# Optimization experiments

Hardware: AMD Instinct MI355X
Metric: run time of the kernel (lower is better)

Reference implementation:

```python
import jax, jax.numpy as jnp
import numpy as np

B, C, H, W = 4, 256, 64, 64
GROUPS = 32
EPS = 1e-5


def setup_inputs() -> dict:
    key = jax.random.key(0)
    ks = jax.random.split(key, 8)
    s = 1.0 / np.sqrt(C)
    return {
        "Hand": jax.random.normal(ks[0], (B, C, H, W), jnp.float32),
        "U": jax.random.normal(ks[1], (B, C, H, W), jnp.float32),
        "WH_w": jax.random.normal(ks[2], (C, C), jnp.float32) * s,
        "WH_b": jax.random.normal(ks[3], (C,), jnp.float32) * 0.01,
        "WU_w": jax.random.normal(ks[4], (C, C), jnp.float32) * s,
        "WU_b": jax.random.normal(ks[5], (C,), jnp.float32) * 0.01,
        "gn_w": jax.random.normal(ks[6], (C,), jnp.float32) * 0.1,
        "gn_b": jax.random.normal(ks[7], (C,), jnp.float32) * 0.1,
    }


def _group_norm(x, w, b):
    # x: [B, C, H, W], normalize within each of GROUPS channel groups over (C//G, H, W)
    b_, c_, h_, w_ = x.shape
    xg = x.reshape(b_, GROUPS, c_ // GROUPS, h_, w_)
    mean = jnp.mean(xg, axis=(2, 3, 4), keepdims=True)
    var = jnp.var(xg, axis=(2, 3, 4), keepdims=True)
    xn = ((xg - mean) * jax.lax.rsqrt(var + EPS)).reshape(b_, c_, h_, w_)
    return xn * w[None, :, None, None] + b[None, :, None, None]


def reference(Hand, U, WH_w, WH_b, WU_w, WU_b, gn_w, gn_b):
    b_, c_, h_, w_ = Hand.shape
    n = h_ * w_
    Hf = Hand.reshape(b_, c_, n)  # [B, C, N]
    Uf = U.reshape(b_, c_, n)     # [B, C, N]
    # 1x1 convs == per-pixel linear on channels
    q = jnp.einsum('oc,bcn->bon', WH_w, Hf) + WH_b[None, :, None]  # [B, C, N]
    k = jnp.einsum('oc,bcn->bon', WU_w, Uf) + WU_b[None, :, None]  # [B, C, N]
    # affinity: A[b, n, m] = sum_c q[b,c,n] * k[b,c,m]  (unscaled)
    A = jnp.einsum('bcn,bcm->bnm', q, k)  # [B, N, N]
    A = jax.nn.softmax(A, axis=-1)
    out = jnp.einsum('bnm,bcm->bcn', A, Uf).reshape(b_, c_, h_, w_)
    return _group_norm(out, gn_w, gn_b) + Hand
```

## Files before the change

### kernel.cpp

```cpp
#include <hip/hip_runtime.h>
#include <hip/hip_fp16.h>
#include <math.h>


typedef _Float16 v8h __attribute__((ext_vector_type(8)));
typedef float    v4f __attribute__((ext_vector_type(4)));

#define NB 4
#define NC 256
#define NS 4096
#define NG 32
#define GEPS 1e-5f
#define NSPLIT 3
#define KSTRIDE 272
#define KTILE   8704
#define PSTRIDE 40

#define ASYNC_BARRIER() asm volatile("s_waitcnt lgkmcnt(0)\n\ts_barrier" ::: "memory")

template <int CTRL>
__device__ __forceinline__ float dpp_rot(float x) {
    int r = __builtin_amdgcn_update_dpp(__float_as_int(x), __float_as_int(x),
                                        CTRL, 0xF, 0xF, false);
    return __int_as_float(r);
}
__device__ __forceinline__ float row_max16(float x) {
    x = fmaxf(x, dpp_rot<0x128>(x));
    x = fmaxf(x, dpp_rot<0x124>(x));
    x = fmaxf(x, dpp_rot<0x122>(x));
    x = fmaxf(x, dpp_rot<0x121>(x));
    return x;
}
__device__ __forceinline__ float row_sum16(float x) {
    x = x + dpp_rot<0x128>(x);
    x = x + dpp_rot<0x124>(x);
    x = x + dpp_rot<0x122>(x);
    x = x + dpp_rot<0x121>(x);
    return x;
}

__global__ __launch_bounds__(256) void k_convert(const float* __restrict__ Wh,
    const float* __restrict__ Wu, _Float16* __restrict__ Wh16, _Float16* __restrict__ Wu16)
{
    const int i = blockIdx.x * 256 + threadIdx.x;
    const int o = i >> 8, c = i & 255;
    const int idx = ((((o >> 4) * 8 + (c >> 5)) * 4 + ((c >> 3) & 3)) * 16
                     + (o & 15)) * 8 + (c & 7);
    Wh16[idx] = (_Float16)Wh[i];
    Wu16[idx] = (_Float16)Wu[i];
}

__global__ __launch_bounds__(256) void k_qkgemm(const float* __restrict__ Hand,
    const float* __restrict__ U, const _Float16* __restrict__ Wh16,
    const _Float16* __restrict__ Wu16, const float* __restrict__ WHb,
    const float* __restrict__ WUb, _Float16* __restrict__ qT,
    _Float16* __restrict__ kTsw, _Float16* __restrict__ Uh)
{
    const int nt = blockIdx.x, b = blockIdx.y, z = blockIdx.z;
    const float*    X    = z ? U    : Hand;
    const _Float16* W    = z ? Wu16 : Wh16;
    const float*    bias = z ? WUb  : WHb;

    const int tid = threadIdx.x, w = tid >> 6, lane = tid & 63;
    const int q4 = lane >> 4, l15 = lane & 15;
    const int n = nt * 64 + w * 16 + l15;

    const float* Xcol = X + (size_t)b * NC * NS + n;
    v8h A[8];
#pragma unroll
    for (int kc = 0; kc < 8; ++kc) {
        const int c0 = kc * 32 + q4 * 8;
        v8h a;
#pragma unroll
        for (int j = 0; j < 8; ++j) a[j] = (_Float16)Xcol[(size_t)(c0 + j) * NS];
        A[kc] = a;
    }

    if (z == 1) {
        _Float16* ub = Uh + (size_t)b * NC * NS + n;
#pragma unroll
        for (int kc = 0; kc < 8; ++kc) {
            const int c0 = kc * 32 + q4 * 8;
#pragma unroll
            for (int j = 0; j < 8; ++j) ub[(size_t)(c0 + j) * NS] = A[kc][j];
        }
    }

#pragma unroll 4
    for (int osub = 0; osub < 16; ++osub) {
        const int o = osub * 16 + l15;
        v4f acc = {0.f, 0.f, 0.f, 0.f};
#pragma unroll
        for (int kc = 0; kc < 8; ++kc) {
            const v8h bf = *(const v8h*)(W + ((size_t)(osub * 8 + kc) * 64 + lane) * 8);
            acc = __builtin_amdgcn_mfma_f32_16x16x32_f16(A[kc], bf, acc, 0, 0, 0);
        }
        const float bv = bias[o];
        if (z == 0) {
            _Float16* orow = qT + ((size_t)b * NS + nt * 64 + w * 16 + q4 * 4) * NC + o;
#pragma unroll
            for (int r = 0; r < 4; ++r) orow[(size_t)r * NC] = (_Float16)(acc[r] + bv);
        } else {
            _Float16* kb = kTsw + (size_t)b * 128 * KTILE;
#pragma unroll
            for (int r = 0; r < 4; ++r) {
                const int m = nt * 64 + w * 16 + q4 * 4 + r;
                kb[(size_t)(m >> 5) * KTILE + (m & 31) * KSTRIDE + o] = (_Float16)(acc[r] + bv);
            }
        }
    }
}

__global__ __launch_bounds__(256, 3) void k_attn(const _Float16* __restrict__ qT,
    const _Float16* __restrict__ kTsw, const _Float16* __restrict__ Uh,
    _Float16* __restrict__ Ppart, float* __restrict__ mstat, float* __restrict__ lstat)
{
    const int b  = blockIdx.x;
    const int nt = blockIdx.y;
    const int s  = blockIdx.z;
    const int t0 = (s == 0) ? 0 : (s == 1 ? 43 : 86);
    const int t1 = (s == 2) ? 128 : t0 + 43;

    __shared__ __align__(16) _Float16 Klds[2][KTILE];
    __shared__ __align__(16) _Float16 Plds[64 * PSTRIDE];
    __shared__ __align__(16) float alphaS[64];

    const int tid = threadIdx.x, w = tid >> 6, lane = tid & 63;
    const int q4 = lane >> 4, l15 = lane & 15;

    const _Float16* kTb = kTsw + (size_t)b * 128 * KTILE;
    const _Float16* Uhb = Uh + (size_t)b * NC * NS;

    {
        const _Float16* src = kTb + (size_t)t0 * KTILE;
#pragma unroll
        for (int j = 0; j < 5; ++j) {
            const int ch = (w * 5 + j) % 17;
            __builtin_amdgcn_global_load_lds(
                (const __attribute__((address_space(1))) void*)(src + ch * 512 + lane * 8),
                (__attribute__((address_space(3))) void*)(&Klds[t0 & 1][ch * 512]), 16, 0, 0);
        }
    }

    v8h Q[8];
    {
        const _Float16* qrow = qT + ((size_t)b * NS + nt * 64 + w * 16 + l15) * NC;
#pragma unroll
        for (int kc = 0; kc < 8; ++kc) Q[kc] = *(const v8h*)(qrow + kc * 32 + q4 * 8);
    }

    v4f O[4][4];
#pragma unroll
    for (int i = 0; i < 4; ++i)
#pragma unroll
        for (int j = 0; j < 4; ++j) O[i][j] = (v4f){0.f, 0.f, 0.f, 0.f};
    float mi[4] = {-INFINITY, -INFINITY, -INFINITY, -INFINITY};
    float li[4] = {0.f, 0.f, 0.f, 0.f};

    for (int t = t0; t < t1; ++t) {
        const int p = t & 1;
        const int m0 = t * 32;

        v8h Ur[4];
#pragma unroll
        for (int js = 0; js < 4; ++js)
            Ur[js] = *(const v8h*)(Uhb + (size_t)(w * 64 + js * 16 + l15) * NS + m0 + q4 * 8);
        asm volatile("" ::: "memory");

        {
            const int tn = (t + 1 < t1) ? t + 1 : t0;
            const _Float16* src = kTb + (size_t)tn * KTILE;
#pragma unroll
            for (int j = 0; j < 5; ++j) {
                const int ch = (w * 5 + j) % 17;
                __builtin_amdgcn_global_load_lds(
                    (const __attribute__((address_space(1))) void*)(src + ch * 512 + lane * 8),
                    (__attribute__((address_space(3))) void*)(&Klds[p ^ 1][ch * 512]), 16, 0, 0);
            }
        }

        asm volatile("s_waitcnt vmcnt(9)" ::: "memory");
        ASYNC_BARRIER();

        v4f sv[2];
        sv[0] = (v4f){0.f, 0.f, 0.f, 0.f};
        sv[1] = (v4f){0.f, 0.f, 0.f, 0.f};
#pragma unroll
        for (int kc = 0; kc < 8; ++kc) {
#pragma unroll
            for (int ms = 0; ms < 2; ++ms) {
                const v8h kf = *(const v8h*)(&Klds[p][(ms * 16 + l15) * KSTRIDE
                                             + (kc * 4 + q4) * 8]);
                sv[ms] = __builtin_amdgcn_mfma_f32_16x16x32_f16(Q[kc], kf, sv[ms], 0, 0, 0);
            }
        }

        float al[4];
#pragma unroll
        for (int r = 0; r < 4; ++r) {
            const float tm = row_max16(fmaxf(sv[0][r], sv[1][r]));
            const float mn = fmaxf(mi[r], tm);
            al[r] = __expf(mi[r] - mn);
            mi[r] = mn;
            const float p0 = __expf(sv[0][r] - mn);
            const float p1 = __expf(sv[1][r] - mn);
            sv[0][r] = p0; sv[1][r] = p1;
            li[r] = li[r] * al[r] + p0 + p1;
        }
        if (l15 == 0) {
#pragma unroll
            for (int r = 0; r < 4; ++r) alphaS[w * 16 + q4 * 4 + r] = al[r];
        }
#pragma unroll
        for (int ms = 0; ms < 2; ++ms)
#pragma unroll
            for (int r = 0; r < 4; ++r) {
                const int row = w * 16 + q4 * 4 + r;
                Plds[row * PSTRIDE + ms * 16 + l15] = (_Float16)sv[ms][r];
            }
        ASYNC_BARRIER();

#pragma unroll
        for (int is = 0; is < 4; ++is) {
            const float4 av = *(const float4*)&alphaS[is * 16 + q4 * 4];
            const v4f aa = {av.x, av.y, av.z, av.w};
#pragma unroll
            for (int js = 0; js < 4; ++js) O[is][js] *= aa;
        }
#pragma unroll
        for (int is = 0; is < 4; ++is) {
            const v8h Pf = *(const v8h*)(&Plds[(is * 16 + l15) * PSTRIDE + q4 * 8]);
#pragma unroll
            for (int js = 0; js < 4; ++js)
                O[is][js] = __builtin_amdgcn_mfma_f32_16x16x32_f16(Pf, Ur[js], O[is][js], 0, 0, 0);
        }
    }

    asm volatile("s_waitcnt vmcnt(0)" ::: "memory");

#pragma unroll
    for (int r = 0; r < 4; ++r) li[r] = row_sum16(li[r]);
    if (l15 == 0) {
#pragma unroll
        for (int r = 0; r < 4; ++r) {
            const int n = nt * 64 + w * 16 + q4 * 4 + r;
            mstat[(size_t)(s * NB + b) * NS + n] = mi[r];
            lstat[(size_t)(s * NB + b) * NS + n] = li[r];
        }
    }
#pragma unroll
    for (int is = 0; is < 4; ++is)
#pragma unroll
        for (int js = 0; js < 4; ++js)
#pragma unroll
            for (int r = 0; r < 4; ++r) {
                _Float16* dst = Ppart + ((size_t)(s * NB + b) * NS + nt * 64 + is * 16
                                         + q4 * 4 + r) * NC + w * 64 + js * 16 + l15;
                __builtin_nontemporal_store((_Float16)O[is][js][r], dst);
            }
}

__global__ __launch_bounds__(256) void k_merge(const _Float16* __restrict__ Pp,
    const float* __restrict__ mstat, const float* __restrict__ lstat,
    float* __restrict__ Opre, float* __restrict__ statacc)
{
    const int b = blockIdx.y, tid = threadIdx.x;
    const int n = blockIdx.x * 8 + (tid >> 5);
    const int c0 = (tid & 31) * 8;
    const size_t nb = (size_t)b * NS + n;
    const size_t SP = (size_t)NB * NS;
    const float m0 = mstat[nb], m1 = mstat[SP + nb], m2 = mstat[2 * SP + nb];
    const float l0 = lstat[nb], l1 = lstat[SP + nb], l2 = lstat[2 * SP + nb];
    const float M  = fmaxf(m0, fmaxf(m1, m2));
    const float e0 = __expf(m0 - M), e1 = __expf(m1 - M), e2 = __expf(m2 - M);
    const float inv = 1.f / (e0 * l0 + e1 * l1 + e2 * l2);
    const float w0 = e0 * inv, w1 = e1 * inv, w2 = e2 * inv;
    const size_t base = nb * NC + c0;
    const v8h p0 = *(const v8h*)(Pp + base);
    const v8h p1 = *(const v8h*)(Pp + SP * NC + base);
    const v8h p2 = *(const v8h*)(Pp + 2 * SP * NC + base);
    float v[8];
    float s1 = 0.f, s2 = 0.f;
#pragma unroll
    for (int j = 0; j < 8; ++j) {
        v[j] = w0 * (float)p0[j] + w1 * (float)p1[j] + w2 * (float)p2[j];
        s1 += v[j]; s2 += v[j] * v[j];
    }
    *(float4*)(Opre + base)     = make_float4(v[0], v[1], v[2], v[3]);
    *(float4*)(Opre + base + 4) = make_float4(v[4], v[5], v[6], v[7]);

    __shared__ float r1[256], r2[256];
    r1[tid] = s1; r2[tid] = s2;
    __syncthreads();
    if (tid < 32) {
        float a = 0.f, q = 0.f;
#pragma unroll
        for (int k = 0; k < 8; ++k) { a += r1[tid + 32 * k]; q += r2[tid + 32 * k]; }
        atomicAdd(&statacc[(b * NG + tid) * 2 + 0], a);
        atomicAdd(&statacc[(b * NG + tid) * 2 + 1], q);
    }
}

__global__ __launch_bounds__(256) void k_gnapply(const float* __restrict__ Opre,
    const float* __restrict__ Hand, const float* __restrict__ gnw,
    const float* __restrict__ gnb, const float* __restrict__ statacc,
    float* __restrict__ out)
{
    const int nt = blockIdx.x, ct = blockIdx.y, b = blockIdx.z;
    __shared__ float buf[64 * 65];
    const int tid = threadIdx.x;
    {
        const int nr = tid >> 4, c4 = (tid & 15) * 4;
#pragma unroll
        for (int k = 0; k < 4; ++k) {
            const int n = nr + 16 * k;
            const float4 v = *(const float4*)(Opre + ((size_t)b * NS + nt * 64 + n) * NC
                                              + ct * 64 + c4);
            buf[n * 65 + c4 + 0] = v.x; buf[n * 65 + c4 + 1] = v.y;
            buf[n * 65 + c4 + 2] = v.z; buf[n * 65 + c4 + 3] = v.w;
        }
    }
    __syncthreads();
    const int nw = tid & 63, c0 = tid >> 6;
#pragma unroll
    for (int k = 0; k < 16; ++k) {
        const int cl = c0 + 4 * k;
        const int c  = ct * 64 + cl;
        const int g  = c >> 3;
        const float s1   = statacc[(b * NG + g) * 2 + 0];
        const float s2   = statacc[(b * NG + g) * 2 + 1];
        const float mean = s1 * (1.f / 32768.f);
        const float var  = s2 * (1.f / 32768.f) - mean * mean;
        const float rstd = rsqrtf(var + GEPS);
        const size_t oidx = ((size_t)b * NC + c) * NS + nt * 64 + nw;
        out[oidx] = (buf[nw * 65 + cl] - mean) * rstd * gnw[c] + gnb[c] + Hand[oidx];
    }
}

extern "C" void kernel_launch(void* const* d_in, const int* in_sizes, int n_in,
                              void* d_out, int out_size, void* d_ws, size_t ws_size,
                              hipStream_t stream)
{
    const float* Hand = (const float*)d_in[0];
    const float* U    = (const float*)d_in[1];
    const float* WHw  = (const float*)d_in[2];
    const float* WHb  = (const float*)d_in[3];
    const float* WUw  = (const float*)d_in[4];
    const float* WUb  = (const float*)d_in[5];
    const float* gnw  = (const float*)d_in[6];
    const float* gnb  = (const float*)d_in[7];
    float* out = (float*)d_out;

    char* ws = (char*)d_ws;
    _Float16* qT     = (_Float16*)(ws);
    _Float16* kTsw   = (_Float16*)(ws + 8388608);
    _Float16* Uh     = (_Float16*)(ws + 17301504);
    _Float16* Wh16   = (_Float16*)(ws + 25690112);
    _Float16* Wu16   = (_Float16*)(ws + 25821184);
    float*    mstat  = (float*)(ws + 25952256);
    float*    lstat  = (float*)(ws + 26148864);
    float*    statacc= (float*)(ws + 26345472);
    _Float16* Ppart  = (_Float16*)(ws + 26347520);
    float*    Opre   = (float*)(ws);

    hipMemsetAsync(statacc, 0, NB * NG * 2 * sizeof(float), stream);
    k_convert<<<dim3((NC * NC) / 256), 256, 0, stream>>>(WHw, WUw, Wh16, Wu16);
    k_qkgemm <<<dim3(64, NB, 2), 256, 0, stream>>>(Hand, U, Wh16, Wu16, WHb, WUb, qT, kTsw, Uh);
    k_attn   <<<dim3(NB, 64, NSPLIT), 256, 0, stream>>>(qT, kTsw, Uh, Ppart, mstat, lstat);
    k_merge  <<<dim3(NS / 8, NB), 256, 0, stream>>>(Ppart, mstat, lstat, Opre, statacc);
    k_gnapply<<<dim3(64, 4, NB), 256, 0, stream>>>(Opre, Hand, gnw, gnb, statacc, out);
}
```

Baseline: 276.1 us.

## Restructure attention pipeline, halve qkgemm blocks, merge output in fp16 in place

The attention loop now double-buffers P and alpha, prefetches K two tiles ahead after the second barrier, and drops one barrier per iteration. It also skips the O rescale when no row max changed. The q/k GEMM launches 128-thread blocks over twice as many tiles to raise parallelism. The merge kernel writes its result as fp16 back into the partial buffer instead of an fp32 Opre array, which cuts memory traffic in the group-norm pass at some cost in precision.

```diff
diff --git a/kernel.cpp b/kernel.cpp
--- a/kernel.cpp
+++ b/kernel.cpp
@@ -4,6 +4,7 @@
 
 
 typedef _Float16 v8h __attribute__((ext_vector_type(8)));
+typedef _Float16 v4h __attribute__((ext_vector_type(4)));
 typedef float    v4f __attribute__((ext_vector_type(4)));
 
 #define NB 4
@@ -50,7 +51,7 @@
     Wu16[idx] = (_Float16)Wu[i];
 }
 
-__global__ __launch_bounds__(256) void k_qkgemm(const float* __restrict__ Hand,
+__global__ __launch_bounds__(128) void k_qkgemm(const float* __restrict__ Hand,
     const float* __restrict__ U, const _Float16* __restrict__ Wh16,
     const _Float16* __restrict__ Wu16, const float* __restrict__ WHb,
     const float* __restrict__ WUb, _Float16* __restrict__ qT,
@@ -63,7 +64,7 @@
 
     const int tid = threadIdx.x, w = tid >> 6, lane = tid & 63;
     const int q4 = lane >> 4, l15 = lane & 15;
-    const int n = nt * 64 + w * 16 + l15;
+    const int n = nt * 32 + w * 16 + l15;
 
     const float* Xcol = X + (size_t)b * NC * NS + n;
     v8h A[8];
@@ -97,14 +98,14 @@
         }
         const float bv = bias[o];
         if (z == 0) {
-            _Float16* orow = qT + ((size_t)b * NS + nt * 64 + w * 16 + q4 * 4) * NC + o;
+            _Float16* orow = qT + ((size_t)b * NS + nt * 32 + w * 16 + q4 * 4) * NC + o;
 #pragma unroll
             for (int r = 0; r < 4; ++r) orow[(size_t)r * NC] = (_Float16)(acc[r] + bv);
         } else {
             _Float16* kb = kTsw + (size_t)b * 128 * KTILE;
 #pragma unroll
             for (int r = 0; r < 4; ++r) {
-                const int m = nt * 64 + w * 16 + q4 * 4 + r;
+                const int m = nt * 32 + w * 16 + q4 * 4 + r;
                 kb[(size_t)(m >> 5) * KTILE + (m & 31) * KSTRIDE + o] = (_Float16)(acc[r] + bv);
             }
         }
@@ -122,8 +123,8 @@
     const int t1 = (s == 2) ? 128 : t0 + 43;
 
     __shared__ __align__(16) _Float16 Klds[2][KTILE];
-    __shared__ __align__(16) _Float16 Plds[64 * PSTRIDE];
-    __shared__ __align__(16) float alphaS[64];
+    __shared__ __align__(16) _Float16 Plds[2][64 * PSTRIDE];
+    __shared__ __align__(16) float alphaS[2][64];
 
     const int tid = threadIdx.x, w = tid >> 6, lane = tid & 63;
     const int q4 = lane >> 4, l15 = lane & 15;
@@ -131,6 +132,13 @@
     const _Float16* kTb = kTsw + (size_t)b * 128 * KTILE;
     const _Float16* Uhb = Uh + (size_t)b * NC * NS;
 
+    v8h Q[8];
+    {
+        const _Float16* qrow = qT + ((size_t)b * NS + nt * 64 + w * 16 + l15) * NC;
+#pragma unroll
+        for (int kc = 0; kc < 8; ++kc) Q[kc] = *(const v8h*)(qrow + kc * 32 + q4 * 8);
+    }
+    asm volatile("s_waitcnt vmcnt(0)" ::: "memory");
     {
         const _Float16* src = kTb + (size_t)t0 * KTILE;
 #pragma unroll
@@ -141,12 +149,17 @@
                 (__attribute__((address_space(3))) void*)(&Klds[t0 & 1][ch * 512]), 16, 0, 0);
         }
     }
-
-    v8h Q[8];
+    asm volatile("s_waitcnt vmcnt(0)" ::: "memory");
+    ASYNC_BARRIER();
     {
-        const _Float16* qrow = qT + ((size_t)b * NS + nt * 64 + w * 16 + l15) * NC;
-#pragma unroll
-        for (int kc = 0; kc < 8; ++kc) Q[kc] = *(const v8h*)(qrow + kc * 32 + q4 * 8);
+        const _Float16* src = kTb + (size_t)(t0 + 1) * KTILE;
+#pragma unroll
+        for (int j = 0; j < 5; ++j) {
+            const int ch = (w * 5 + j) % 17;
+            __builtin_amdgcn_global_load_lds(
+                (const __attribute__((address_space(1))) void*)(src + ch * 512 + lane * 8),
+                (__attribute__((address_space(3))) void*)(&Klds[(t0 + 1) & 1][ch * 512]), 16, 0, 0);
+        }
     }
 
     v4f O[4][4];
@@ -165,22 +178,6 @@
 #pragma unroll
         for (int js = 0; js < 4; ++js)
             Ur[js] = *(const v8h*)(Uhb + (size_t)(w * 64 + js * 16 + l15) * NS + m0 + q4 * 8);
-        asm volatile("" ::: "memory");
-
-        {
-            const int tn = (t + 1 < t1) ? t + 1 : t0;
-            const _Float16* src = kTb + (size_t)tn * KTILE;
-#pragma unroll
-            for (int j = 0; j < 5; ++j) {
-                const int ch = (w * 5 + j) % 17;
-                __builtin_amdgcn_global_load_lds(
-                    (const __attribute__((address_space(1))) void*)(src + ch * 512 + lane * 8),
-                    (__attribute__((address_space(3))) void*)(&Klds[p ^ 1][ch * 512]), 16, 0, 0);
-            }
-        }
-
-        asm volatile("s_waitcnt vmcnt(9)" ::: "memory");
-        ASYNC_BARRIER();
 
         v4f sv[2];
         sv[0] = (v4f){0.f, 0.f, 0.f, 0.f};
@@ -209,27 +206,51 @@
         }
         if (l15 == 0) {
 #pragma unroll
-            for (int r = 0; r < 4; ++r) alphaS[w * 16 + q4 * 4 + r] = al[r];
+            for (int r = 0; r < 4; ++r) alphaS[p][w * 16 + q4 * 4 + r] = al[r];
         }
 #pragma unroll
         for (int ms = 0; ms < 2; ++ms)
 #pragma unroll
             for (int r = 0; r < 4; ++r) {
                 const int row = w * 16 + q4 * 4 + r;
-                Plds[row * PSTRIDE + ms * 16 + l15] = (_Float16)sv[ms][r];
-            }
+                Plds[p][row * PSTRIDE + ms * 16 + l15] = (_Float16)sv[ms][r];
+            }
+
+        asm volatile("s_waitcnt vmcnt(4)" ::: "memory");
         ASYNC_BARRIER();
 
+        {
+            const int tn = (t + 2 < t1) ? t + 2 : t0;
+            const _Float16* src = kTb + (size_t)tn * KTILE;
+#pragma unroll
+            for (int j = 0; j < 5; ++j) {
+                const int ch = (w * 5 + j) % 17;
+                __builtin_amdgcn_global_load_lds(
+                    (const __attribute__((address_space(1))) void*)(src + ch * 512 + lane * 8),
+                    (__attribute__((address_space(3))) void*)(&Klds[p][ch * 512]), 16, 0, 0);
+            }
+        }
+
+        float4 av[4];
+#pragma unroll
+        for (int is = 0; is < 4; ++is)
+            av[is] = *(const float4*)&alphaS[p][is * 16 + q4 * 4];
+        bool need = false;
+#pragma unroll
+        for (int is = 0; is < 4; ++is)
+            need |= (av[is].x < 1.f) | (av[is].y < 1.f) | (av[is].z < 1.f) | (av[is].w < 1.f);
+        if (__ballot(need)) {
+#pragma unroll
+            for (int is = 0; is < 4; ++is) {
+                const v4f aa = {av[is].x, av[is].y, av[is].z, av[is].w};
+#pragma unroll
+                for (int js = 0; js < 4; ++js) O[is][js] *= aa;
+            }
+        }
+
 #pragma unroll
         for (int is = 0; is < 4; ++is) {
-            const float4 av = *(const float4*)&alphaS[is * 16 + q4 * 4];
-            const v4f aa = {av.x, av.y, av.z, av.w};
-#pragma unroll
-            for (int js = 0; js < 4; ++js) O[is][js] *= aa;
-        }
-#pragma unroll
-        for (int is = 0; is < 4; ++is) {
-            const v8h Pf = *(const v8h*)(&Plds[(is * 16 + l15) * PSTRIDE + q4 * 8]);
+            const v8h Pf = *(const v8h*)(&Plds[p][(is * 16 + l15) * PSTRIDE + q4 * 8]);
 #pragma unroll
             for (int js = 0; js < 4; ++js)
                 O[is][js] = __builtin_amdgcn_mfma_f32_16x16x32_f16(Pf, Ur[js], O[is][js], 0, 0, 0);
@@ -260,9 +281,9 @@
             }
 }
 
-__global__ __launch_bounds__(256) void k_merge(const _Float16* __restrict__ Pp,
+__global__ __launch_bounds__(256) void k_merge(_Float16* __restrict__ Pp,
     const float* __restrict__ mstat, const float* __restrict__ lstat,
-    float* __restrict__ Opre, float* __restrict__ statacc)
+    float* __restrict__ statacc)
 {
     const int b = blockIdx.y, tid = threadIdx.x;
     const int n = blockIdx.x * 8 + (tid >> 5);
@@ -279,15 +300,15 @@
     const v8h p0 = *(const v8h*)(Pp + base);
     const v8h p1 = *(const v8h*)(Pp + SP * NC + base);
     const v8h p2 = *(const v8h*)(Pp + 2 * SP * NC + base);
-    float v[8];
     float s1 = 0.f, s2 = 0.f;
+    v8h hm;
 #pragma unroll
     for (int j = 0; j < 8; ++j) {
-        v[j] = w0 * (float)p0[j] + w1 * (float)p1[j] + w2 * (float)p2[j];
-        s1 += v[j]; s2 += v[j] * v[j];
-    }
-    *(float4*)(Opre + base)     = make_float4(v[0], v[1], v[2], v[3]);
-    *(float4*)(Opre + base + 4) = make_float4(v[4], v[5], v[6], v[7]);
+        const float v = w0 * (float)p0[j] + w1 * (float)p1[j] + w2 * (float)p2[j];
+        s1 += v; s2 += v * v;
+        hm[j] = (_Float16)v;
+    }
+    *(v8h*)(Pp + base) = hm;
 
     __shared__ float r1[256], r2[256];
     r1[tid] = s1; r2[tid] = s2;
@@ -301,7 +322,7 @@
     }
 }
 
-__global__ __launch_bounds__(256) void k_gnapply(const float* __restrict__ Opre,
+__global__ __launch_bounds__(256) void k_gnapply(const _Float16* __restrict__ Om,
     const float* __restrict__ Hand, const float* __restrict__ gnw,
     const float* __restrict__ gnb, const float* __restrict__ statacc,
     float* __restrict__ out)
@@ -314,10 +335,10 @@
 #pragma unroll
         for (int k = 0; k < 4; ++k) {
             const int n = nr + 16 * k;
-            const float4 v = *(const float4*)(Opre + ((size_t)b * NS + nt * 64 + n) * NC
-                                              + ct * 64 + c4);
-            buf[n * 65 + c4 + 0] = v.x; buf[n * 65 + c4 + 1] = v.y;
-            buf[n * 65 + c4 + 2] = v.z; buf[n * 65 + c4 + 3] = v.w;
+            const v4h v = *(const v4h*)(Om + ((size_t)b * NS + nt * 64 + n) * NC
+                                        + ct * 64 + c4);
+            buf[n * 65 + c4 + 0] = (float)v[0]; buf[n * 65 + c4 + 1] = (float)v[1];
+            buf[n * 65 + c4 + 2] = (float)v[2]; buf[n * 65 + c4 + 3] = (float)v[3];
         }
     }
     __syncthreads();
@@ -361,12 +382,11 @@
     float*    lstat  = (float*)(ws + 26148864);
     float*    statacc= (float*)(ws + 26345472);
     _Float16* Ppart  = (_Float16*)(ws + 26347520);
-    float*    Opre   = (float*)(ws);
 
     hipMemsetAsync(statacc, 0, NB * NG * 2 * sizeof(float), stream);
     k_convert<<<dim3((NC * NC) / 256), 256, 0, stream>>>(WHw, WUw, Wh16, Wu16);
-    k_qkgemm <<<dim3(64, NB, 2), 256, 0, stream>>>(Hand, U, Wh16, Wu16, WHb, WUb, qT, kTsw, Uh);
+    k_qkgemm <<<dim3(128, NB, 2), 128, 0, stream>>>(Hand, U, Wh16, Wu16, WHb, WUb, qT, kTsw, Uh);
     k_attn   <<<dim3(NB, 64, NSPLIT), 256, 0, stream>>>(qT, kTsw, Uh, Ppart, mstat, lstat);
-    k_merge  <<<dim3(NS / 8, NB), 256, 0, stream>>>(Ppart, mstat, lstat, Opre, statacc);
-    k_gnapply<<<dim3(64, 4, NB), 256, 0, stream>>>(Opre, Hand, gnw, gnb, statacc, out);
-}
+    k_merge  <<<dim3(NS / 8, NB), 256, 0, stream>>>(Ppart, mstat, lstat, statacc);
+    k_gnapply<<<dim3(64, 4, NB), 256, 0, stream>>>(Ppart, Hand, gnw, gnb, statacc, out);
+}
```

Result: no change. 278.6 us (+0.9%).
